# Kernel optimization log

Measured on AMD Instinct MI355X. Metric: run time of the kernel, lower is better.

Reference implementation:

```python
import jax, jax.numpy as jnp
import numpy as np

V, D = 100000, 128
B, Q, C, T = 1024, 64, 64, 8


def setup_inputs() -> dict:
    key = jax.random.key(0)
    ks = jax.random.split(key, 9)
    embed = jax.random.normal(ks[0], (V, D), dtype=jnp.float32) * 0.1
    embed = embed.at[0].set(0.0)  # padding_idx=0
    q_ids = jax.random.randint(ks[1], (B, Q), 1, V)
    c_ids = jax.random.randint(ks[2], (B, C, T), 1, V)
    num_qs = jax.random.randint(ks[3], (B,), 1, Q + 1)
    num_cols = jax.random.randint(ks[4], (B,), 1, C + 1)
    W_h = jax.random.normal(ks[5], (5 * D, D), dtype=jnp.float32) * 0.02
    b_h = jnp.zeros((D,), jnp.float32)
    W_o = jax.random.normal(ks[6], (D, 1), dtype=jnp.float32) * 0.02
    b_o = jnp.zeros((1,), jnp.float32)
    return {"q_ids": q_ids, "c_ids": c_ids, "num_qs": num_qs, "num_cols": num_cols,
            "embed": embed, "W_h": W_h, "b_h": b_h, "W_o": W_o, "b_o": b_o}


def _forward(q_ids, c_ids, num_qs, num_cols, embed, W_h, b_h, W_o, b_o):
    d = embed.shape[1]
    # ColumnSummarizer: pad-masked mean over column tokens -> [B, C, D]
    c_tok = embed[c_ids]                       # [B, C, T, D]
    c_mask = (c_ids != 0).astype(c_tok.dtype)  # [B, C, T]
    denom = jnp.maximum(c_mask.sum(-1, keepdims=True), 1.0)
    c_h = (c_tok * c_mask[..., None]).sum(-2) / denom  # [B, C, D]
    # QuestionSummarizer: q_h = token embeddings, q_summary = length-masked mean
    q_h = embed[q_ids]                         # [B, Q, D]
    q_valid = (jnp.arange(q_h.shape[1])[None, :] < num_qs[:, None])  # [B, Q]
    qv = q_valid.astype(q_h.dtype)
    q_summary = (q_h * qv[..., None]).sum(1) / jnp.maximum(
        num_qs[:, None].astype(q_h.dtype), 1.0)  # [B, D]
    # scaled dot-product attention, columns attend over question tokens
    sim = jnp.einsum('bcd,bqd->bcq', c_h, q_h) / jnp.sqrt(jnp.asarray(d, c_h.dtype))
    sim = jnp.where(q_valid[:, None, :], sim, -jnp.inf)  # mask padded q tokens
    att = jax.nn.softmax(sim, axis=-1)                    # [B, C, Q]
    weighted_q = jnp.einsum('bcq,bqd->bcd', att, q_h)     # [B, C, D]
    q_tiled = jnp.broadcast_to(q_summary[:, None, :], c_h.shape)
    feats = jnp.concatenate(
        [q_tiled, c_h, weighted_q, c_h * weighted_q, jnp.abs(c_h - weighted_q)],
        axis=-1)                                           # [B, C, 5D]
    h = jnp.tanh(feats @ W_h + b_h)
    return h @ W_o + b_o                                   # [B, C, 1]


def reference(q_ids, c_ids, num_qs, num_cols, embed, W_h, b_h, W_o, b_o):
    return _forward(q_ids, c_ids, num_qs, num_cols, embed, W_h, b_h, W_o, b_o)
```

## Files before the change

### kernel.cpp

```cpp
#include <hip/hip_runtime.h>


typedef __attribute__((ext_vector_type(8))) short     short8;
typedef __attribute__((ext_vector_type(8))) __bf16    bf16x8;
typedef __attribute__((ext_vector_type(4))) float     f32x4;

#define SWZ(row, off) ((off) ^ (((row) & 7) << 4))

#define CH_OFF    0
#define QH_OFF    16384
#define QHT_OFF   32768
#define X_OFF     49152
#define IDS_C     (X_OFF)
#define IDS_Q     (X_OFF + 2048)
#define QSP_OFF   (X_OFF)
#define QSUM_OFF  (X_OFF + 1024)
#define OUTP_OFF  (X_OFF + 1280)
#define LDS_SIZE  (X_OFF + 2304)

__device__ __forceinline__ unsigned short f2bf(float x) {
    unsigned u = __builtin_bit_cast(unsigned, x);
    u += 0x7FFFu + ((u >> 16) & 1u);
    return (unsigned short)(u >> 16);
}
__device__ __forceinline__ float bf2f(unsigned short u) {
    return __builtin_bit_cast(float, ((unsigned)u) << 16);
}
__device__ __forceinline__ float bflo(unsigned u) {
    return __builtin_bit_cast(float, u << 16);
}
__device__ __forceinline__ float bfhi(unsigned u) {
    return __builtin_bit_cast(float, u & 0xFFFF0000u);
}
__device__ __forceinline__ f32x4 mfma16(short8 a, short8 b, f32x4 c) {
    return __builtin_amdgcn_mfma_f32_16x16x32_bf16(
        __builtin_bit_cast(bf16x8, a), __builtin_bit_cast(bf16x8, b), c, 0, 0, 0);
}

__global__ __launch_bounds__(256) void el_prep(const float* __restrict__ W_h,
                                               unsigned short* __restrict__ whT) {
    int t = blockIdx.x * 256 + threadIdx.x;
    int k = t >> 7, n = t & 127;
    whT[n * 640 + k] = f2bf(W_h[t]);
}

__global__ __launch_bounds__(256) void el_conv(const float* __restrict__ e,
                                               unsigned short* __restrict__ ebf) {
    long i = ((long)blockIdx.x * 256 + threadIdx.x) * 8;
    f32x4 a = *(const f32x4*)(e + i);
    f32x4 c = *(const f32x4*)(e + i + 4);
    uint4 pk;
    pk.x = (unsigned)f2bf(a[0]) | ((unsigned)f2bf(a[1]) << 16);
    pk.y = (unsigned)f2bf(a[2]) | ((unsigned)f2bf(a[3]) << 16);
    pk.z = (unsigned)f2bf(c[0]) | ((unsigned)f2bf(c[1]) << 16);
    pk.w = (unsigned)f2bf(c[2]) | ((unsigned)f2bf(c[3]) << 16);
    *(uint4*)(ebf + i) = pk;
}

template <bool BF16E>
__global__ __launch_bounds__(256, 3) void el_main(
    const int* __restrict__ q_ids, const int* __restrict__ c_ids,
    const int* __restrict__ num_qs, const float* __restrict__ emb,
    const unsigned short* __restrict__ ebf,
    const unsigned short* __restrict__ whT, const float* __restrict__ b_h,
    const float* __restrict__ W_o, const float* __restrict__ b_o,
    float* __restrict__ out)
{
    __shared__ __align__(16) char smem[LDS_SIZE];
    const int tid = threadIdx.x;
    const int b = blockIdx.x;
    const int nq = num_qs[b] > 0 ? num_qs[b] : 1;

    {
        int* idc = (int*)(smem + IDS_C);
        idc[tid]       = c_ids[(b << 9) + tid];
        idc[tid + 256] = c_ids[(b << 9) + tid + 256];
        if (tid < 64) ((int*)(smem + IDS_Q))[tid] = q_ids[(b << 6) + tid];
    }
    __syncthreads();

    if constexpr (BF16E) {
        const int l4 = tid & 15, gg = tid >> 4;
        #pragma unroll 2
        for (int cc = 0; cc < 4; ++cc) {
            const int c = gg + cc * 16;
            const int* idp = (const int*)(smem + IDS_C) + c * 8;
            int id8[8];
            #pragma unroll
            for (int t = 0; t < 8; ++t) id8[t] = idp[t];
            float acc[8] = {0.f,0.f,0.f,0.f,0.f,0.f,0.f,0.f};
            int cnt = 0;
            #pragma unroll
            for (int t = 0; t < 8; ++t) {
                uint4 v = *(const uint4*)(ebf + (long)id8[t] * 128 + l4 * 8);
                cnt += (id8[t] != 0);
                acc[0] += bflo(v.x); acc[1] += bfhi(v.x);
                acc[2] += bflo(v.y); acc[3] += bfhi(v.y);
                acc[4] += bflo(v.z); acc[5] += bfhi(v.z);
                acc[6] += bflo(v.w); acc[7] += bfhi(v.w);
            }
            float inv = 1.0f / (float)(cnt > 0 ? cnt : 1);
            uint4 pk;
            pk.x = (unsigned)f2bf(acc[0]*inv) | ((unsigned)f2bf(acc[1]*inv) << 16);
            pk.y = (unsigned)f2bf(acc[2]*inv) | ((unsigned)f2bf(acc[3]*inv) << 16);
            pk.z = (unsigned)f2bf(acc[4]*inv) | ((unsigned)f2bf(acc[5]*inv) << 16);
            pk.w = (unsigned)f2bf(acc[6]*inv) | ((unsigned)f2bf(acc[7]*inv) << 16);
            *(uint4*)(smem + CH_OFF + SWZ(c, c * 256 + l4 * 16)) = pk;
        }
        #pragma unroll
        for (int qq = 0; qq < 4; ++qq) {
            const int q = gg + qq * 16;
            int id = ((const int*)(smem + IDS_Q))[q];
            uint4 v = *(const uint4*)(ebf + (long)id * 128 + l4 * 8);
            *(uint4*)(smem + QH_OFF + SWZ(q, q * 256 + l4 * 16)) = v;
        }
    } else {
        const int l = tid & 31, g = tid >> 5;
        #pragma unroll 2
        for (int cc = 0; cc < 8; ++cc) {
            const int c = g + cc * 8;
            const int* idp = (const int*)(smem + IDS_C) + c * 8;
            int id8[8];
            #pragma unroll
            for (int t = 0; t < 8; ++t) id8[t] = idp[t];
            f32x4 acc = {0.f, 0.f, 0.f, 0.f};
            int cnt = 0;
            #pragma unroll
            for (int t = 0; t < 8; ++t) {
                f32x4 v = *(const f32x4*)(emb + (long)id8[t] * 128 + l * 4);
                cnt += (id8[t] != 0);
                acc += v;
            }
            float inv = 1.0f / (float)(cnt > 0 ? cnt : 1);
            uint2 pk;
            pk.x = (unsigned)f2bf(acc[0]*inv) | ((unsigned)f2bf(acc[1]*inv) << 16);
            pk.y = (unsigned)f2bf(acc[2]*inv) | ((unsigned)f2bf(acc[3]*inv) << 16);
            *(uint2*)(smem + CH_OFF + SWZ(c, c * 256 + l * 8)) = pk;
        }
        #pragma unroll
        for (int qq = 0; qq < 8; ++qq) {
            const int q = g + qq * 8;
            int id = ((const int*)(smem + IDS_Q))[q];
            f32x4 v = *(const f32x4*)(emb + (long)id * 128 + l * 4);
            uint2 pk;
            pk.x = (unsigned)f2bf(v[0]) | ((unsigned)f2bf(v[1]) << 16);
            pk.y = (unsigned)f2bf(v[2]) | ((unsigned)f2bf(v[3]) << 16);
            *(uint2*)(smem + QH_OFF + SWZ(q, q * 256 + l * 8)) = pk;
        }
    }
    __syncthreads();

    {
        const int d = tid >> 1, qh = (tid & 1) * 32;
        unsigned v16[32];
        #pragma unroll
        for (int j = 0; j < 32; ++j) {
            int q = qh + j;
            v16[j] = *(const unsigned short*)(smem + QH_OFF + SWZ(q, q * 256 + d * 2));
        }
        #pragma unroll
        for (int i = 0; i < 4; ++i) {
            uint4 pk;
            pk.x = v16[i*8+0] | (v16[i*8+1] << 16);
            pk.y = v16[i*8+2] | (v16[i*8+3] << 16);
            pk.z = v16[i*8+4] | (v16[i*8+5] << 16);
            pk.w = v16[i*8+6] | (v16[i*8+7] << 16);
            *(uint4*)(smem + QHT_OFF + SWZ(d, d * 128 + qh * 2 + i * 16)) = pk;
        }
        const int d2 = tid & 127, h = tid >> 7;
        float s = 0.f;
        #pragma unroll
        for (int j = 0; j < 32; ++j) {
            int q = h * 32 + j;
            float v = bf2f(*(const unsigned short*)(smem + QH_OFF + SWZ(q, q * 256 + d2 * 2)));
            s += (q < nq) ? v : 0.f;
        }
        ((float*)(smem + QSP_OFF))[h * 128 + d2] = s;
    }
    __syncthreads();

    const int lane = tid & 63, w = tid >> 6;
    const int lr = lane & 15, lg = lane >> 4;

    float attv[4][4];
    {
        short8 a[4];
        const int arow = w * 16 + lr;
        #pragma unroll
        for (int s = 0; s < 4; ++s)
            a[s] = *(const short8*)(smem + CH_OFF + SWZ(arow, arow * 256 + s * 64 + lg * 16));
        f32x4 sim[4];
        #pragma unroll
        for (int ct = 0; ct < 4; ++ct) {
            f32x4 acc = {0.f, 0.f, 0.f, 0.f};
            const int q = ct * 16 + lr;
            #pragma unroll
            for (int s = 0; s < 4; ++s) {
                short8 bf = *(const short8*)(smem + QH_OFF + SWZ(q, q * 256 + s * 64 + lg * 16));
                acc = mfma16(a[s], bf, acc);
            }
            sim[ct] = acc;
        }
        const float scale = 0.08838834764831845f;
        #pragma unroll
        for (int ct = 0; ct < 4; ++ct) {
            const int q = ct * 16 + lr;
            #pragma unroll
            for (int r = 0; r < 4; ++r)
                sim[ct][r] = (q < nq) ? sim[ct][r] * scale : -3.0e38f;
        }
        float mx[4], sm[4];
        #pragma unroll
        for (int r = 0; r < 4; ++r)
            mx[r] = fmaxf(fmaxf(sim[0][r], sim[1][r]), fmaxf(sim[2][r], sim[3][r]));
        #pragma unroll
        for (int off = 1; off <= 8; off <<= 1)
            #pragma unroll
            for (int r = 0; r < 4; ++r)
                mx[r] = fmaxf(mx[r], __shfl_xor(mx[r], off));
        #pragma unroll
        for (int ct = 0; ct < 4; ++ct)
            #pragma unroll
            for (int r = 0; r < 4; ++r)
                sim[ct][r] = __expf(sim[ct][r] - mx[r]);
        #pragma unroll
        for (int r = 0; r < 4; ++r)
            sm[r] = (sim[0][r] + sim[1][r]) + (sim[2][r] + sim[3][r]);
        #pragma unroll
        for (int off = 1; off <= 8; off <<= 1)
            #pragma unroll
            for (int r = 0; r < 4; ++r)
                sm[r] += __shfl_xor(sm[r], off);
        #pragma unroll
        for (int ct = 0; ct < 4; ++ct)
            #pragma unroll
            for (int r = 0; r < 4; ++r)
                attv[ct][r] = sim[ct][r] * (1.0f / sm[r]);
    }
    __syncthreads();
    {
        const int cbase = w * 16 + lg * 4;
        #pragma unroll
        for (int ct = 0; ct < 4; ++ct)
            #pragma unroll
            for (int r = 0; r < 4; ++r) {
                int c = cbase + r, q = ct * 16 + lr;
                *(unsigned short*)(smem + QH_OFF + SWZ(c, c * 128 + q * 2)) =
                    f2bf(attv[ct][r]);
            }
        if (tid < 128) {
            const float* qsp = (const float*)(smem + QSP_OFF);
            float s = (qsp[tid] + qsp[128 + tid]) / (float)nq;
            *(unsigned short*)(smem + QSUM_OFF + tid * 2) = f2bf(s);
        }
    }
    __syncthreads();

    f32x4 wqa[8];
    {
        short8 pa[2];
        const int prow = w * 16 + lr;
        #pragma unroll
        for (int s = 0; s < 2; ++s)
            pa[s] = *(const short8*)(smem + QH_OFF + SWZ(prow, prow * 128 + s * 64 + lg * 16));
        #pragma unroll
        for (int ct = 0; ct < 8; ++ct) {
            f32x4 acc = {0.f, 0.f, 0.f, 0.f};
            const int dcol = ct * 16 + lr;
            #pragma unroll
            for (int s = 0; s < 2; ++s) {
                short8 bf = *(const short8*)(smem + QHT_OFF + SWZ(dcol, dcol * 128 + s * 64 + lg * 16));
                acc = mfma16(pa[s], bf, acc);
            }
            wqa[ct] = acc;
        }
    }
    __syncthreads();
    {
        const int cbase = w * 16 + lg * 4;
        #pragma unroll
        for (int ct = 0; ct < 8; ++ct)
            #pragma unroll
            for (int r = 0; r < 4; ++r) {
                int c = cbase + r, d = ct * 16 + lr;
                *(unsigned short*)(smem + QH_OFF + SWZ(c, c * 256 + d * 2)) = f2bf(wqa[ct][r]);
            }
    }
    __syncthreads();

    {
        f32x4 acc[4][2];
        #pragma unroll
        for (int rt = 0; rt < 4; ++rt) {
            acc[rt][0] = (f32x4){0.f, 0.f, 0.f, 0.f};
            acc[rt][1] = (f32x4){0.f, 0.f, 0.f, 0.f};
        }
        const int n0 = w * 32 + lr, n1 = n0 + 16;

        for (int sk = 0; sk < 4; ++sk) {
            short8 B0[5], B1[5];
            #pragma unroll
            for (int p = 0; p < 5; ++p) {
                B0[p] = *(const short8*)(whT + n0 * 640 + p * 128 + sk * 32 + lg * 8);
                B1[p] = *(const short8*)(whT + n1 * 640 + p * 128 + sk * 32 + lg * 8);
            }
            short8 qsf = *(const short8*)(smem + QSUM_OFF + sk * 64 + lg * 16);
            #pragma unroll
            for (int rt = 0; rt < 4; ++rt) {
                const int row = rt * 16 + lr;
                short8 chf = *(const short8*)(smem + CH_OFF + SWZ(row, row * 256 + sk * 64 + lg * 16));
                short8 wqf = *(const short8*)(smem + QH_OFF + SWZ(row, row * 256 + sk * 64 + lg * 16));
                short8 prf, adf;
                #pragma unroll
                for (int e = 0; e < 8; ++e) {
                    float cv = bf2f((unsigned short)chf[e]);
                    float wv = bf2f((unsigned short)wqf[e]);
                    prf[e] = (short)f2bf(cv * wv);
                    adf[e] = (short)f2bf(fabsf(cv - wv));
                }
                acc[rt][0] = mfma16(qsf, B0[0], acc[rt][0]);
                acc[rt][1] = mfma16(qsf, B1[0], acc[rt][1]);
                acc[rt][0] = mfma16(chf, B0[1], acc[rt][0]);
                acc[rt][1] = mfma16(chf, B1[1], acc[rt][1]);
                acc[rt][0] = mfma16(wqf, B0[2], acc[rt][0]);
                acc[rt][1] = mfma16(wqf, B1[2], acc[rt][1]);
                acc[rt][0] = mfma16(prf, B0[3], acc[rt][0]);
                acc[rt][1] = mfma16(prf, B1[3], acc[rt][1]);
                acc[rt][0] = mfma16(adf, B0[4], acc[rt][0]);
                acc[rt][1] = mfma16(adf, B1[4], acc[rt][1]);
            }
        }

        float bh0 = b_h[n0], bh1 = b_h[n1];
        float wo0 = W_o[n0], wo1 = W_o[n1];
        #pragma unroll
        for (int rt = 0; rt < 4; ++rt)
            #pragma unroll
            for (int r = 0; r < 4; ++r) {
                float x0 = acc[rt][0][r] + bh0;
                float x1 = acc[rt][1][r] + bh1;
                float t0 = 1.0f - 2.0f / (__expf(2.0f * x0) + 1.0f);
                float t1 = 1.0f - 2.0f / (__expf(2.0f * x1) + 1.0f);
                float po = t0 * wo0 + t1 * wo1;
                #pragma unroll
                for (int off = 1; off <= 8; off <<= 1)
                    po += __shfl_xor(po, off);
                if (lr == 0)
                    *(float*)(smem + OUTP_OFF + (w * 64 + rt * 16 + lg * 4 + r) * 4) = po;
            }
    }
    __syncthreads();

    if (tid < 64) {
        float o = b_o[0];
        #pragma unroll
        for (int w2 = 0; w2 < 4; ++w2)
            o += *(const float*)(smem + OUTP_OFF + (w2 * 64 + tid) * 4);
        out[(b << 6) + tid] = o;
    }
}

extern "C" void kernel_launch(void* const* d_in, const int* in_sizes, int n_in,
                              void* d_out, int out_size, void* d_ws, size_t ws_size,
                              hipStream_t stream) {
    const int*   q_ids  = (const int*)d_in[0];
    const int*   c_ids  = (const int*)d_in[1];
    const int*   num_qs = (const int*)d_in[2];
    const float* embed  = (const float*)d_in[4];
    const float* W_h    = (const float*)d_in[5];
    const float* b_h    = (const float*)d_in[6];
    const float* W_o    = (const float*)d_in[7];
    const float* b_o    = (const float*)d_in[8];
    float*       out    = (float*)d_out;

    unsigned short* whT = (unsigned short*)d_ws;
    unsigned short* ebf = (unsigned short*)d_ws + 81920;

    el_prep<<<320, 256, 0, stream>>>(W_h, whT);

    const bool bf16e = ws_size >= (size_t)(163840 + 100000 * 128 * 2);
    if (bf16e) {
        el_conv<<<6250, 256, 0, stream>>>(embed, ebf);
        el_main<true><<<1024, 256, 0, stream>>>(q_ids, c_ids, num_qs, embed, ebf,
                                                whT, b_h, W_o, b_o, out);
    } else {
        el_main<false><<<1024, 256, 0, stream>>>(q_ids, c_ids, num_qs, embed, ebf,
                                                 whT, b_h, W_o, b_o, out);
    }
}
```

Measured before the change: 158.6 us.

## Shrink LDS footprint, drop transposed Q copy, restructure final GEMM per-wave rows

Removes the transposed QH buffer and the staging of ids in shared memory. Q and column ids are read directly from global memory, the question summary is folded into the gather loop, and the summary is staged through a workspace buffer. LDS use drops from about 51KB to 40KB, and launch bounds are raised to 4 blocks per CU to increase occupancy. The final hidden GEMM now gives each wave its own 16 rows across all 128 outputs and writes results directly, which removes one shared-memory round trip and a barrier. The trade-offs are scalar strided LDS reads in the weighted-Q MFMA, more global reads of whT per wave, and higher register pressure under the tighter bound.

```diff
diff --git a/kernel.cpp b/kernel.cpp
--- a/kernel.cpp
+++ b/kernel.cpp
@@ -4,24 +4,19 @@
 typedef __attribute__((ext_vector_type(8))) short     short8;
 typedef __attribute__((ext_vector_type(8))) __bf16    bf16x8;
 typedef __attribute__((ext_vector_type(4))) float     f32x4;
-
-#define SWZ(row, off) ((off) ^ (((row) & 7) << 4))
-
-#define CH_OFF    0
-#define QH_OFF    16384
-#define QHT_OFF   32768
-#define X_OFF     49152
-#define IDS_C     (X_OFF)
-#define IDS_Q     (X_OFF + 2048)
-#define QSP_OFF   (X_OFF)
-#define QSUM_OFF  (X_OFF + 1024)
-#define OUTP_OFF  (X_OFF + 1280)
-#define LDS_SIZE  (X_OFF + 2304)
+typedef __attribute__((ext_vector_type(4))) int       int4v;
+
+#define SWZ8(row, off) ((off) ^ (((row) & 7) << 4))
+#define SWZQ(row, off) ((off) ^ (((row) & 7) << 4) ^ ((((row) >> 3) & 3) << 5))
+
+#define CH_OFF  0
+#define QH_OFF  16384
+#define SC_OFF  32768
+#define LDS_SIZE 40960
 
 __device__ __forceinline__ unsigned short f2bf(float x) {
-    unsigned u = __builtin_bit_cast(unsigned, x);
-    u += 0x7FFFu + ((u >> 16) & 1u);
-    return (unsigned short)(u >> 16);
+    __bf16 h = (__bf16)x;
+    return __builtin_bit_cast(unsigned short, h);
 }
 __device__ __forceinline__ float bf2f(unsigned short u) {
     return __builtin_bit_cast(float, ((unsigned)u) << 16);
@@ -31,6 +26,9 @@
 }
 __device__ __forceinline__ float bfhi(unsigned u) {
     return __builtin_bit_cast(float, u & 0xFFFF0000u);
+}
+__device__ __forceinline__ unsigned pk2(float a, float b) {
+    return (unsigned)f2bf(a) | ((unsigned)f2bf(b) << 16);
 }
 __device__ __forceinline__ f32x4 mfma16(short8 a, short8 b, f32x4 c) {
     return __builtin_amdgcn_mfma_f32_16x16x32_bf16(
@@ -50,19 +48,19 @@
     f32x4 a = *(const f32x4*)(e + i);
     f32x4 c = *(const f32x4*)(e + i + 4);
     uint4 pk;
-    pk.x = (unsigned)f2bf(a[0]) | ((unsigned)f2bf(a[1]) << 16);
-    pk.y = (unsigned)f2bf(a[2]) | ((unsigned)f2bf(a[3]) << 16);
-    pk.z = (unsigned)f2bf(c[0]) | ((unsigned)f2bf(c[1]) << 16);
-    pk.w = (unsigned)f2bf(c[2]) | ((unsigned)f2bf(c[3]) << 16);
+    pk.x = pk2(a[0], a[1]); pk.y = pk2(a[2], a[3]);
+    pk.z = pk2(c[0], c[1]); pk.w = pk2(c[2], c[3]);
     *(uint4*)(ebf + i) = pk;
 }
 
 template <bool BF16E>
-__global__ __launch_bounds__(256, 3) void el_main(
+__global__ __launch_bounds__(256, 4) void el_main(
     const int* __restrict__ q_ids, const int* __restrict__ c_ids,
     const int* __restrict__ num_qs, const float* __restrict__ emb,
     const unsigned short* __restrict__ ebf,
-    const unsigned short* __restrict__ whT, const float* __restrict__ b_h,
+    const unsigned short* __restrict__ whT,
+    unsigned short* __restrict__ qsum_ws,
+    const float* __restrict__ b_h,
     const float* __restrict__ W_o, const float* __restrict__ b_o,
     float* __restrict__ out)
 {
@@ -72,123 +70,84 @@
     const int nq = num_qs[b] > 0 ? num_qs[b] : 1;
 
     {
-        int* idc = (int*)(smem + IDS_C);
-        idc[tid]       = c_ids[(b << 9) + tid];
-        idc[tid + 256] = c_ids[(b << 9) + tid + 256];
-        if (tid < 64) ((int*)(smem + IDS_Q))[tid] = q_ids[(b << 6) + tid];
-    }
-    __syncthreads();
-
-    if constexpr (BF16E) {
         const int l4 = tid & 15, gg = tid >> 4;
         #pragma unroll 2
         for (int cc = 0; cc < 4; ++cc) {
             const int c = gg + cc * 16;
-            const int* idp = (const int*)(smem + IDS_C) + c * 8;
-            int id8[8];
-            #pragma unroll
-            for (int t = 0; t < 8; ++t) id8[t] = idp[t];
+            const int* idp = c_ids + (((b << 6) + c) << 3);
+            int4v i0 = *(const int4v*)idp, i1 = *(const int4v*)(idp + 4);
+            int id8[8] = {i0[0], i0[1], i0[2], i0[3], i1[0], i1[1], i1[2], i1[3]};
+            int cnt = 0;
+            #pragma unroll
+            for (int t = 0; t < 8; ++t) cnt += (id8[t] != 0);
             float acc[8] = {0.f,0.f,0.f,0.f,0.f,0.f,0.f,0.f};
-            int cnt = 0;
             #pragma unroll
             for (int t = 0; t < 8; ++t) {
-                uint4 v = *(const uint4*)(ebf + (long)id8[t] * 128 + l4 * 8);
-                cnt += (id8[t] != 0);
-                acc[0] += bflo(v.x); acc[1] += bfhi(v.x);
-                acc[2] += bflo(v.y); acc[3] += bfhi(v.y);
-                acc[4] += bflo(v.z); acc[5] += bfhi(v.z);
-                acc[6] += bflo(v.w); acc[7] += bfhi(v.w);
+                if constexpr (BF16E) {
+                    uint4 v = *(const uint4*)(ebf + (long)id8[t] * 128 + l4 * 8);
+                    acc[0] += bflo(v.x); acc[1] += bfhi(v.x);
+                    acc[2] += bflo(v.y); acc[3] += bfhi(v.y);
+                    acc[4] += bflo(v.z); acc[5] += bfhi(v.z);
+                    acc[6] += bflo(v.w); acc[7] += bfhi(v.w);
+                } else {
+                    f32x4 lo = *(const f32x4*)(emb + (long)id8[t] * 128 + l4 * 8);
+                    f32x4 hi = *(const f32x4*)(emb + (long)id8[t] * 128 + l4 * 8 + 4);
+                    acc[0] += lo[0]; acc[1] += lo[1]; acc[2] += lo[2]; acc[3] += lo[3];
+                    acc[4] += hi[0]; acc[5] += hi[1]; acc[6] += hi[2]; acc[7] += hi[3];
+                }
             }
             float inv = 1.0f / (float)(cnt > 0 ? cnt : 1);
             uint4 pk;
-            pk.x = (unsigned)f2bf(acc[0]*inv) | ((unsigned)f2bf(acc[1]*inv) << 16);
-            pk.y = (unsigned)f2bf(acc[2]*inv) | ((unsigned)f2bf(acc[3]*inv) << 16);
-            pk.z = (unsigned)f2bf(acc[4]*inv) | ((unsigned)f2bf(acc[5]*inv) << 16);
-            pk.w = (unsigned)f2bf(acc[6]*inv) | ((unsigned)f2bf(acc[7]*inv) << 16);
-            *(uint4*)(smem + CH_OFF + SWZ(c, c * 256 + l4 * 16)) = pk;
-        }
+            pk.x = pk2(acc[0]*inv, acc[1]*inv); pk.y = pk2(acc[2]*inv, acc[3]*inv);
+            pk.z = pk2(acc[4]*inv, acc[5]*inv); pk.w = pk2(acc[6]*inv, acc[7]*inv);
+            *(uint4*)(smem + CH_OFF + SWZ8(c, c * 256 + l4 * 16)) = pk;
+        }
+        float qa[8] = {0.f,0.f,0.f,0.f,0.f,0.f,0.f,0.f};
         #pragma unroll
         for (int qq = 0; qq < 4; ++qq) {
-            const int q = gg + qq * 16;
-            int id = ((const int*)(smem + IDS_Q))[q];
-            uint4 v = *(const uint4*)(ebf + (long)id * 128 + l4 * 8);
-            *(uint4*)(smem + QH_OFF + SWZ(q, q * 256 + l4 * 16)) = v;
-        }
-    } else {
-        const int l = tid & 31, g = tid >> 5;
-        #pragma unroll 2
-        for (int cc = 0; cc < 8; ++cc) {
-            const int c = g + cc * 8;
-            const int* idp = (const int*)(smem + IDS_C) + c * 8;
-            int id8[8];
-            #pragma unroll
-            for (int t = 0; t < 8; ++t) id8[t] = idp[t];
-            f32x4 acc = {0.f, 0.f, 0.f, 0.f};
-            int cnt = 0;
-            #pragma unroll
-            for (int t = 0; t < 8; ++t) {
-                f32x4 v = *(const f32x4*)(emb + (long)id8[t] * 128 + l * 4);
-                cnt += (id8[t] != 0);
-                acc += v;
-            }
-            float inv = 1.0f / (float)(cnt > 0 ? cnt : 1);
-            uint2 pk;
-            pk.x = (unsigned)f2bf(acc[0]*inv) | ((unsigned)f2bf(acc[1]*inv) << 16);
-            pk.y = (unsigned)f2bf(acc[2]*inv) | ((unsigned)f2bf(acc[3]*inv) << 16);
-            *(uint2*)(smem + CH_OFF + SWZ(c, c * 256 + l * 8)) = pk;
-        }
-        #pragma unroll
-        for (int qq = 0; qq < 8; ++qq) {
-            const int q = g + qq * 8;
-            int id = ((const int*)(smem + IDS_Q))[q];
-            f32x4 v = *(const f32x4*)(emb + (long)id * 128 + l * 4);
-            uint2 pk;
-            pk.x = (unsigned)f2bf(v[0]) | ((unsigned)f2bf(v[1]) << 16);
-            pk.y = (unsigned)f2bf(v[2]) | ((unsigned)f2bf(v[3]) << 16);
-            *(uint2*)(smem + QH_OFF + SWZ(q, q * 256 + l * 8)) = pk;
-        }
-    }
-    __syncthreads();
-
-    {
-        const int d = tid >> 1, qh = (tid & 1) * 32;
-        unsigned v16[32];
-        #pragma unroll
-        for (int j = 0; j < 32; ++j) {
-            int q = qh + j;
-            v16[j] = *(const unsigned short*)(smem + QH_OFF + SWZ(q, q * 256 + d * 2));
-        }
-        #pragma unroll
-        for (int i = 0; i < 4; ++i) {
-            uint4 pk;
-            pk.x = v16[i*8+0] | (v16[i*8+1] << 16);
-            pk.y = v16[i*8+2] | (v16[i*8+3] << 16);
-            pk.z = v16[i*8+4] | (v16[i*8+5] << 16);
-            pk.w = v16[i*8+6] | (v16[i*8+7] << 16);
-            *(uint4*)(smem + QHT_OFF + SWZ(d, d * 128 + qh * 2 + i * 16)) = pk;
-        }
-        const int d2 = tid & 127, h = tid >> 7;
+            const int q = gg + (qq << 4);
+            int id = q_ids[(b << 6) + q];
+            uint4 v;
+            if constexpr (BF16E) {
+                v = *(const uint4*)(ebf + (long)id * 128 + l4 * 8);
+            } else {
+                f32x4 lo = *(const f32x4*)(emb + (long)id * 128 + l4 * 8);
+                f32x4 hi = *(const f32x4*)(emb + (long)id * 128 + l4 * 8 + 4);
+                v.x = pk2(lo[0], lo[1]); v.y = pk2(lo[2], lo[3]);
+                v.z = pk2(hi[0], hi[1]); v.w = pk2(hi[2], hi[3]);
+            }
+            *(uint4*)(smem + QH_OFF + SWZQ(q, q * 256 + l4 * 16)) = v;
+            if (q < nq) {
+                qa[0] += bflo(v.x); qa[1] += bfhi(v.x);
+                qa[2] += bflo(v.y); qa[3] += bfhi(v.y);
+                qa[4] += bflo(v.z); qa[5] += bfhi(v.z);
+                qa[6] += bflo(v.w); qa[7] += bfhi(v.w);
+            }
+        }
+        float* qsp = (float*)(smem + SC_OFF);
+        *(f32x4*)(qsp + gg * 128 + l4 * 8)     = (f32x4){qa[0], qa[1], qa[2], qa[3]};
+        *(f32x4*)(qsp + gg * 128 + l4 * 8 + 4) = (f32x4){qa[4], qa[5], qa[6], qa[7]};
+    }
+    __syncthreads();
+
+    if (tid < 128) {
+        const float* qsp = (const float*)(smem + SC_OFF);
         float s = 0.f;
         #pragma unroll
-        for (int j = 0; j < 32; ++j) {
-            int q = h * 32 + j;
-            float v = bf2f(*(const unsigned short*)(smem + QH_OFF + SWZ(q, q * 256 + d2 * 2)));
-            s += (q < nq) ? v : 0.f;
-        }
-        ((float*)(smem + QSP_OFF))[h * 128 + d2] = s;
+        for (int g = 0; g < 16; ++g) s += qsp[g * 128 + tid];
+        qsum_ws[(b << 7) + tid] = f2bf(s / (float)nq);
     }
     __syncthreads();
 
     const int lane = tid & 63, w = tid >> 6;
     const int lr = lane & 15, lg = lane >> 4;
 
-    float attv[4][4];
     {
         short8 a[4];
         const int arow = w * 16 + lr;
         #pragma unroll
         for (int s = 0; s < 4; ++s)
-            a[s] = *(const short8*)(smem + CH_OFF + SWZ(arow, arow * 256 + s * 64 + lg * 16));
+            a[s] = *(const short8*)(smem + CH_OFF + SWZ8(arow, arow * 256 + s * 64 + lg * 16));
         f32x4 sim[4];
         #pragma unroll
         for (int ct = 0; ct < 4; ++ct) {
@@ -196,7 +155,7 @@
             const int q = ct * 16 + lr;
             #pragma unroll
             for (int s = 0; s < 4; ++s) {
-                short8 bf = *(const short8*)(smem + QH_OFF + SWZ(q, q * 256 + s * 64 + lg * 16));
+                short8 bf = *(const short8*)(smem + QH_OFF + SWZQ(q, q * 256 + s * 64 + lg * 16));
                 acc = mfma16(a[s], bf, acc);
             }
             sim[ct] = acc;
@@ -231,49 +190,45 @@
             #pragma unroll
             for (int r = 0; r < 4; ++r)
                 sm[r] += __shfl_xor(sm[r], off);
-        #pragma unroll
-        for (int ct = 0; ct < 4; ++ct)
-            #pragma unroll
-            for (int r = 0; r < 4; ++r)
-                attv[ct][r] = sim[ct][r] * (1.0f / sm[r]);
-    }
-    __syncthreads();
-    {
         const int cbase = w * 16 + lg * 4;
         #pragma unroll
         for (int ct = 0; ct < 4; ++ct)
             #pragma unroll
             for (int r = 0; r < 4; ++r) {
                 int c = cbase + r, q = ct * 16 + lr;
-                *(unsigned short*)(smem + QH_OFF + SWZ(c, c * 128 + q * 2)) =
-                    f2bf(attv[ct][r]);
-            }
-        if (tid < 128) {
-            const float* qsp = (const float*)(smem + QSP_OFF);
-            float s = (qsp[tid] + qsp[128 + tid]) / (float)nq;
-            *(unsigned short*)(smem + QSUM_OFF + tid * 2) = f2bf(s);
-        }
+                *(unsigned short*)(smem + SC_OFF + SWZ8(c, c * 128 + q * 2)) =
+                    f2bf(sim[ct][r] * (1.0f / sm[r]));
+            }
     }
     __syncthreads();
 
     f32x4 wqa[8];
     {
         short8 pa[2];
-        const int prow = w * 16 + lr;
+        const int arow = w * 16 + lr;
         #pragma unroll
         for (int s = 0; s < 2; ++s)
-            pa[s] = *(const short8*)(smem + QH_OFF + SWZ(prow, prow * 128 + s * 64 + lg * 16));
+            pa[s] = *(const short8*)(smem + SC_OFF + SWZ8(arow, arow * 128 + s * 64 + lg * 16));
+        const int d2 = (lr << 1);
         #pragma unroll
         for (int ct = 0; ct < 8; ++ct) {
             f32x4 acc = {0.f, 0.f, 0.f, 0.f};
-            const int dcol = ct * 16 + lr;
+            const int d = ct * 16 + lr;
+            const int dlx = (d << 1) ^ (lg << 5);
             #pragma unroll
             for (int s = 0; s < 2; ++s) {
-                short8 bf = *(const short8*)(smem + QHT_OFF + SWZ(dcol, dcol * 128 + s * 64 + lg * 16));
+                const int qbase = (s << 5) + (lg << 3);
+                short8 bf;
+                #pragma unroll
+                for (int j = 0; j < 8; ++j) {
+                    int off = QH_OFF + ((qbase + j) << 8) + (dlx ^ (j << 4));
+                    bf[j] = *(const short*)(smem + off);
+                }
                 acc = mfma16(pa[s], bf, acc);
             }
             wqa[ct] = acc;
         }
+        (void)d2;
     }
     __syncthreads();
     {
@@ -283,80 +238,72 @@
             #pragma unroll
             for (int r = 0; r < 4; ++r) {
                 int c = cbase + r, d = ct * 16 + lr;
-                *(unsigned short*)(smem + QH_OFF + SWZ(c, c * 256 + d * 2)) = f2bf(wqa[ct][r]);
-            }
-    }
-    __syncthreads();
-
-    {
-        f32x4 acc[4][2];
-        #pragma unroll
-        for (int rt = 0; rt < 4; ++rt) {
-            acc[rt][0] = (f32x4){0.f, 0.f, 0.f, 0.f};
-            acc[rt][1] = (f32x4){0.f, 0.f, 0.f, 0.f};
-        }
-        const int n0 = w * 32 + lr, n1 = n0 + 16;
-
+                *(unsigned short*)(smem + QH_OFF + SWZQ(c, c * 256 + d * 2)) =
+                    f2bf(wqa[ct][r]);
+            }
+    }
+    __syncthreads();
+
+    {
+        f32x4 acc[8];
+        #pragma unroll
+        for (int nt = 0; nt < 8; ++nt) acc[nt] = (f32x4){0.f, 0.f, 0.f, 0.f};
+
+        short8 qsf[4];
+        #pragma unroll
+        for (int sk = 0; sk < 4; ++sk)
+            qsf[sk] = *(const short8*)(qsum_ws + (b << 7) + sk * 32 + lg * 8);
+        float bh[8], wo[8];
+        #pragma unroll
+        for (int nt = 0; nt < 8; ++nt) {
+            bh[nt] = b_h[nt * 16 + lr];
+            wo[nt] = W_o[nt * 16 + lr];
+        }
+        const int row = w * 16 + lr;
+
+        #pragma unroll
         for (int sk = 0; sk < 4; ++sk) {
-            short8 B0[5], B1[5];
-            #pragma unroll
-            for (int p = 0; p < 5; ++p) {
-                B0[p] = *(const short8*)(whT + n0 * 640 + p * 128 + sk * 32 + lg * 8);
-                B1[p] = *(const short8*)(whT + n1 * 640 + p * 128 + sk * 32 + lg * 8);
-            }
-            short8 qsf = *(const short8*)(smem + QSUM_OFF + sk * 64 + lg * 16);
-            #pragma unroll
-            for (int rt = 0; rt < 4; ++rt) {
-                const int row = rt * 16 + lr;
-                short8 chf = *(const short8*)(smem + CH_OFF + SWZ(row, row * 256 + sk * 64 + lg * 16));
-                short8 wqf = *(const short8*)(smem + QH_OFF + SWZ(row, row * 256 + sk * 64 + lg * 16));
-                short8 prf, adf;
-                #pragma unroll
-                for (int e = 0; e < 8; ++e) {
-                    float cv = bf2f((unsigned short)chf[e]);
-                    float wv = bf2f((unsigned short)wqf[e]);
-                    prf[e] = (short)f2bf(cv * wv);
-                    adf[e] = (short)f2bf(fabsf(cv - wv));
-                }
-                acc[rt][0] = mfma16(qsf, B0[0], acc[rt][0]);
-                acc[rt][1] = mfma16(qsf, B1[0], acc[rt][1]);
-                acc[rt][0] = mfma16(chf, B0[1], acc[rt][0]);
-                acc[rt][1] = mfma16(chf, B1[1], acc[rt][1]);
-                acc[rt][0] = mfma16(wqf, B0[2], acc[rt][0]);
-                acc[rt][1] = mfma16(wqf, B1[2], acc[rt][1]);
-                acc[rt][0] = mfma16(prf, B0[3], acc[rt][0]);
-                acc[rt][1] = mfma16(prf, B1[3], acc[rt][1]);
-                acc[rt][0] = mfma16(adf, B0[4], acc[rt][0]);
-                acc[rt][1] = mfma16(adf, B1[4], acc[rt][1]);
-            }
-        }
-
-        float bh0 = b_h[n0], bh1 = b_h[n1];
-        float wo0 = W_o[n0], wo1 = W_o[n1];
-        #pragma unroll
-        for (int rt = 0; rt < 4; ++rt)
+            short8 chf = *(const short8*)(smem + CH_OFF + SWZ8(row, row * 256 + sk * 64 + lg * 16));
+            short8 wqf = *(const short8*)(smem + QH_OFF + SWZQ(row, row * 256 + sk * 64 + lg * 16));
+            short8 prf, adf;
+            #pragma unroll
+            for (int e = 0; e < 8; ++e) {
+                float cv = bf2f((unsigned short)chf[e]);
+                float wv = bf2f((unsigned short)wqf[e]);
+                prf[e] = (short)f2bf(cv * wv);
+                adf[e] = (short)f2bf(fabsf(cv - wv));
+            }
+            const unsigned short* wp = whT + sk * 32 + lg * 8;
+            #pragma unroll
+            for (int nt = 0; nt < 8; ++nt) {
+                const unsigned short* wpn = wp + (nt * 16 + lr) * 640;
+                acc[nt] = mfma16(qsf[sk], *(const short8*)(wpn      ), acc[nt]);
+                acc[nt] = mfma16(chf,     *(const short8*)(wpn + 128), acc[nt]);
+                acc[nt] = mfma16(wqf,     *(const short8*)(wpn + 256), acc[nt]);
+                acc[nt] = mfma16(prf,     *(const short8*)(wpn + 384), acc[nt]);
+                acc[nt] = mfma16(adf,     *(const short8*)(wpn + 512), acc[nt]);
+            }
+        }
+
+        float po[4] = {0.f, 0.f, 0.f, 0.f};
+        #pragma unroll
+        for (int nt = 0; nt < 8; ++nt)
             #pragma unroll
             for (int r = 0; r < 4; ++r) {
-                float x0 = acc[rt][0][r] + bh0;
-                float x1 = acc[rt][1][r] + bh1;
-                float t0 = 1.0f - 2.0f / (__expf(2.0f * x0) + 1.0f);
-                float t1 = 1.0f - 2.0f / (__expf(2.0f * x1) + 1.0f);
-                float po = t0 * wo0 + t1 * wo1;
-                #pragma unroll
-                for (int off = 1; off <= 8; off <<= 1)
-                    po += __shfl_xor(po, off);
-                if (lr == 0)
-                    *(float*)(smem + OUTP_OFF + (w * 64 + rt * 16 + lg * 4 + r) * 4) = po;
-            }
-    }
-    __syncthreads();
-
-    if (tid < 64) {
-        float o = b_o[0];
-        #pragma unroll
-        for (int w2 = 0; w2 < 4; ++w2)
-            o += *(const float*)(smem + OUTP_OFF + (w2 * 64 + tid) * 4);
-        out[(b << 6) + tid] = o;
+                float x = acc[nt][r] + bh[nt];
+                float t = 1.0f - 2.0f / (__expf(2.0f * x) + 1.0f);
+                po[r] += t * wo[nt];
+            }
+        #pragma unroll
+        for (int off = 1; off <= 8; off <<= 1)
+            #pragma unroll
+            for (int r = 0; r < 4; ++r)
+                po[r] += __shfl_xor(po[r], off);
+        if (lr == 0) {
+            float bo = b_o[0];
+            f32x4 o = {po[0] + bo, po[1] + bo, po[2] + bo, po[3] + bo};
+            *(f32x4*)(out + (b << 6) + w * 16 + lg * 4) = o;
+        }
     }
 }
 
@@ -373,18 +320,19 @@
     const float* b_o    = (const float*)d_in[8];
     float*       out    = (float*)d_out;
 
-    unsigned short* whT = (unsigned short*)d_ws;
-    unsigned short* ebf = (unsigned short*)d_ws + 81920;
+    unsigned short* whT  = (unsigned short*)d_ws;
+    unsigned short* qsum = (unsigned short*)((char*)d_ws + 163840);
+    unsigned short* ebf  = (unsigned short*)((char*)d_ws + 425984);
 
     el_prep<<<320, 256, 0, stream>>>(W_h, whT);
 
-    const bool bf16e = ws_size >= (size_t)(163840 + 100000 * 128 * 2);
+    const bool bf16e = ws_size >= (size_t)(425984 + 100000 * 128 * 2);
     if (bf16e) {
         el_conv<<<6250, 256, 0, stream>>>(embed, ebf);
         el_main<true><<<1024, 256, 0, stream>>>(q_ids, c_ids, num_qs, embed, ebf,
-                                                whT, b_h, W_o, b_o, out);
+                                                whT, qsum, b_h, W_o, b_o, out);
     } else {
         el_main<false><<<1024, 256, 0, stream>>>(q_ids, c_ids, num_qs, embed, ebf,
-                                                 whT, b_h, W_o, b_o, out);
-    }
-}
+                                                 whT, qsum, b_h, W_o, b_o, out);
+    }
+}
```

New measurement: 201.8 us. +27.3%, slower.
